# Kernel optimization log

Hardware: AMD Instinct MI355X
Metric: run time of the kernel (lower is better)

The kernel has to match this reference:

```python
import jax, jax.numpy as jnp
import numpy as np

N, C, E, B, NPG, MAX_LEN, H, EF = 16384, 512, 524288, 64, 256, 512, 8, 16
EPS = 1e-5

def layernorm(x, g, b):
    m = jnp.mean(x, axis=-1, keepdims=True)
    v = jnp.mean(jnp.square(x - m), axis=-1, keepdims=True)
    return (x - m) / jnp.sqrt(v + EPS) * g + b

def setup_inputs() -> dict:
    key = jax.random.key(0)
    ks = list(jax.random.split(key, 32))
    x = jax.random.normal(ks[0], (N, C), dtype=jnp.float32)
    edge_attr = jax.random.normal(ks[1], (E, EF), dtype=jnp.float32)
    # edges within each graph of NPG nodes
    src = jax.random.randint(ks[2], (E,), 0, N)
    dst = (src // NPG) * NPG + jax.random.randint(ks[3], (E,), 0, NPG)
    edge_index = jnp.stack([src, dst]).astype(jnp.int64)
    batch = jnp.repeat(jnp.arange(B), NPG).astype(jnp.int64)  # sorted graph ids
    s = 0.03
    p = lambda k, shp: jax.random.normal(k, shp, dtype=jnp.float32) * s
    return dict(
        x=x, edge_attr=edge_attr,
        gcn_w=p(ks[4], (C, C)), gcn_b=jnp.zeros((C,)),
        ep_w=p(ks[5], (EF, C)), ep_b=jnp.zeros((C,)),
        gate_w=p(ks[6], (2 * C, C)), gate_b=jnp.zeros((C,)),
        n1_g=jnp.ones((C,)), n1_b=jnp.zeros((C,)),
        in_w=p(ks[7], (C, 3 * C)), in_b=jnp.zeros((3 * C,)),
        out_w=p(ks[8], (C, C)), out_b=jnp.zeros((C,)),
        tn_g=jnp.ones((C,)), tn_b=jnp.zeros((C,)),
        m_w1=p(ks[9], (C, 2 * C)), m_b1=jnp.zeros((2 * C,)),
        m_w2=p(ks[10], (2 * C, C)), m_b2=jnp.zeros((C,)),
        fn_g=jnp.ones((C,)), fn_b=jnp.zeros((C,)),
        edge_index=edge_index, batch=batch,
    )

def reference(x, edge_attr, gcn_w, gcn_b, ep_w, ep_b, gate_w, gate_b,
              n1_g, n1_b, in_w, in_b, out_w, out_b, tn_g, tn_b,
              m_w1, m_b1, m_w2, m_b2, fn_g, fn_b, edge_index, batch):
    src, dst = edge_index[0], edge_index[1]
    # --- CoGNN: weighted GCN conv (self-loops, sym norm) ---
    ew = jax.lax.stop_gradient(jnp.sqrt(jnp.sum(edge_attr * edge_attr, axis=-1)))
    loop = jnp.arange(N)
    src2 = jnp.concatenate([src, loop]); dst2 = jnp.concatenate([dst, loop])
    ew2 = jnp.concatenate([ew, jnp.ones((N,), ew.dtype)])
    deg = jax.ops.segment_sum(ew2, dst2, num_segments=N)
    dinv = jnp.where(deg > 0, jax.lax.rsqrt(jnp.maximum(deg, 1e-12)), 0.0)
    norm = dinv[src2] * ew2 * dinv[dst2]
    xw = x @ gcn_w
    x_conv = jax.ops.segment_sum(norm[:, None] * xw[src2], dst2, num_segments=N) + gcn_b
    # edge_proj -> scatter_add at source nodes (dropout = identity in eval)
    ef = jax.nn.relu(edge_attr @ ep_w + ep_b)
    ef = jax.ops.segment_sum(ef, src, num_segments=N)
    gate = jax.nn.sigmoid(jnp.concatenate([x_conv, ef], axis=-1) @ gate_w + gate_b)
    x1 = gate * x_conv + (1.0 - gate) * ef
    x1 = jax.nn.relu(layernorm(x1, n1_g, n1_b))
    x = x1 + x  # identity residual (in_channels == hidden_channels)
    # --- to_dense_batch ---
    counts = jax.ops.segment_sum(jnp.ones((N,), jnp.int32), batch, num_segments=B)
    starts = jnp.cumsum(counts) - counts
    pos = jnp.arange(N) - starts[batch]
    xd = jnp.zeros((B, MAX_LEN, C), x.dtype).at[batch, pos].set(x)
    maskd = jnp.zeros((B, MAX_LEN), bool).at[batch, pos].set(True)
    # --- MHA (batch_first, key_padding_mask = ~mask) ---
    Dh = C // H
    qkv = xd @ in_w + in_b
    q, k, v = jnp.split(qkv, 3, axis=-1)
    q = q.reshape(B, MAX_LEN, H, Dh); k = k.reshape(B, MAX_LEN, H, Dh); v = v.reshape(B, MAX_LEN, H, Dh)
    scores = jnp.einsum('blhd,bmhd->bhlm', q, k) / jnp.sqrt(jnp.asarray(Dh, x.dtype))
    scores = jnp.where(maskd[:, None, None, :], scores, -1e9)
    attn = jax.nn.softmax(scores, axis=-1)
    o = jnp.einsum('bhlm,bmhd->blhd', attn, v).reshape(B, MAX_LEN, C)
    o = o @ out_w + out_b
    x_global = o[batch, pos]  # undo dense batching: x_global[mask]
    x = layernorm(x + x_global, tn_g, tn_b)
    # --- MLP ---
    x = x + (jax.nn.silu(x @ m_w1 + m_b1) @ m_w2 + m_b2)
    return layernorm(x, fn_g, fn_b)
```

## Files before the change

kernel.cpp:

```cpp
#include <hip/hip_runtime.h>

#define NN 16384
#define CC 512
#define EE 524288
#define BB 64
#define HH 8
#define EFD 16
#define GEMAXE 10240

typedef __bf16 bf16_t;
typedef __bf16 bf16x4 __attribute__((ext_vector_type(4)));
typedef __bf16 bf16x8 __attribute__((ext_vector_type(8)));
typedef float f32x4v __attribute__((ext_vector_type(4)));

__device__ __forceinline__ float2 ldb2(const bf16_t* p) {
  unsigned w = *(const unsigned*)p;
  return make_float2(__uint_as_float(w << 16), __uint_as_float(w & 0xFFFF0000u));
}

__device__ __forceinline__ int2 xcd_swizzle() {
  int nwg = gridDim.x * gridDim.y;
  int bid = blockIdx.y * gridDim.x + blockIdx.x;
  int wg = (bid & 7) * (nwg >> 3) + (bid >> 3);
  return make_int2(wg % gridDim.x, wg / gridDim.x);
}


__global__ void init_kernel(int* ghist, int* nid_src, bf16_t* eacsr) {
  int i = threadIdx.x;
  if (i < 64) ghist[i] = 0;
  if (i < 32) nid_src[EE + i] = -1;
  ((int*)(eacsr + (size_t)EE * 16))[i] = 0;
}

__global__ __launch_bounds__(256) void edge_pass1(const int* __restrict__ dst,
                                                  int* ghist) {
  __shared__ int h[64];
  int tid = threadIdx.x;
  if (tid < 64) h[tid] = 0;
  __syncthreads();
  int e = blockIdx.x * 256 + tid;
  atomicAdd(&h[dst[e] >> 8], 1);
  __syncthreads();
  if (tid < 64 && h[tid]) atomicAdd(&ghist[tid], h[tid]);
}

__global__ void gexscan_kernel(const int* __restrict__ ghist, int* __restrict__ gstart,
                               int* __restrict__ gcur) {
  if (threadIdx.x == 0) {
    int s = 0;
    for (int g = 0; g < 64; ++g) { gstart[g] = s; gcur[g] = s; s += ghist[g]; }
    gstart[64] = s;
  }
}

__global__ __launch_bounds__(256) void graph_scatter_kernel(
    const int* __restrict__ src, const int* __restrict__ dst,
    const float* __restrict__ ea, int* gcur, int2* __restrict__ grec,
    float* __restrict__ ewg) {
  __shared__ int h[64], base[64], h2[64];
  int tid = threadIdx.x;
  if (tid < 64) { h[tid] = 0; h2[tid] = 0; }
  __syncthreads();
  int e0 = blockIdx.x * 2048;
  int gloc[8];
#pragma unroll
  for (int k = 0; k < 8; ++k) {
    gloc[k] = dst[e0 + k * 256 + tid] >> 8;
    atomicAdd(&h[gloc[k]], 1);
  }
  __syncthreads();
  if (tid < 64) base[tid] = h[tid] ? atomicAdd(&gcur[tid], h[tid]) : 0;
  __syncthreads();
#pragma unroll
  for (int k = 0; k < 8; ++k) {
    int e = e0 + k * 256 + tid;
    int g = gloc[k];
    int p = atomicAdd(&h2[g], 1);
    int pos = base[g] + p;
    int ls = src[e] & 255;
    int ld = dst[e] & 255;
    grec[pos] = make_int2(e | (ls << 19), ld);
    const float4* pa = (const float4*)(ea + (size_t)e * EFD);
    float s = 0.f;
#pragma unroll
    for (int q = 0; q < 4; ++q) {
      float4 v = pa[q];
      s += v.x * v.x + v.y * v.y + v.z * v.z + v.w * v.w;
    }
    ewg[pos] = sqrtf(s);
  }
}

__global__ __launch_bounds__(1024) void graph_sort2_kernel(
    const int2* __restrict__ grec, const float* __restrict__ ewg,
    const int* __restrict__ gstart, int* __restrict__ elist_src,
    int* __restrict__ nid_src, int* __restrict__ start_src,
    float2* __restrict__ dstrec, int* __restrict__ start_dst,
    float* __restrict__ dinv) {
  __shared__ int lbuf[GEMAXE];
  __shared__ unsigned short sl[GEMAXE];
  __shared__ float ewl[GEMAXE];
  __shared__ int h[256], hx[256], h2[256];
  __shared__ float fdinv[256];
  const int g = blockIdx.x & 63;
  const int tid = threadIdx.x;
  const int gs = gstart[g];
  const int cnt = gstart[g + 1] - gs;
  if (tid < 256) { h[tid] = 0; h2[tid] = 0; }
  __syncthreads();
  if (blockIdx.x < 64) {
    for (int i = tid; i < cnt; i += 1024) {
      int2 r = grec[gs + i];
      int ld = r.y;
      sl[i] = (unsigned short)(((r.x >> 19) & 255) | (ld << 8));
      ewl[i] = ewg[gs + i];
      atomicAdd(&h[ld], 1);
    }
    __syncthreads();
    int myc = (tid < 256) ? h[tid] : 0;
    for (int off = 1; off < 256; off <<= 1) {
      int v = (tid < 256 && tid >= off) ? h[tid - off] : 0;
      __syncthreads();
      if (tid < 256) h[tid] += v;
      __syncthreads();
    }
    if (tid < 256) {
      hx[tid] = h[tid] - myc;
      start_dst[g * 256 + tid] = gs + hx[tid];
    }
    if (g == 63 && tid == 0) start_dst[NN] = EE;
    __syncthreads();
    for (int i = tid; i < cnt; i += 1024) {
      int ld = sl[i] >> 8;
      int p = hx[ld] + atomicAdd(&h2[ld], 1);
      lbuf[p] = i;
    }
    __syncthreads();
    if (tid < 256) {
      float dg = 1.0f;
      int s0 = hx[tid], e0 = s0 + myc;
      for (int i = s0; i < e0; ++i) dg += ewl[lbuf[i]];
      float dv = rsqrtf(fmaxf(dg, 1e-12f));
      fdinv[tid] = dv;
      dinv[g * 256 + tid] = dv;
    }
    __syncthreads();
    for (int p = tid; p < cnt; p += 1024) {
      int i = lbuf[p];
      int ls = sl[i] & 255;
      int ld = sl[i] >> 8;
      dstrec[gs + p] =
          make_float2(fdinv[ls] * ewl[i] * fdinv[ld], __int_as_float(ls));
    }
  } else {
    int* wb = (int*)ewl;
    for (int i = tid; i < cnt; i += 1024) {
      int w = grec[gs + i].x;
      wb[i] = w;
      atomicAdd(&h[w >> 19], 1);
    }
    __syncthreads();
    int myc = (tid < 256) ? h[tid] : 0;
    for (int off = 1; off < 256; off <<= 1) {
      int v = (tid < 256 && tid >= off) ? h[tid - off] : 0;
      __syncthreads();
      if (tid < 256) h[tid] += v;
      __syncthreads();
    }
    if (tid < 256) {
      hx[tid] = h[tid] - myc;
      start_src[g * 256 + tid] = gs + hx[tid];
    }
    if (g == 63 && tid == 0) start_src[NN] = EE;
    __syncthreads();
    for (int i = tid; i < cnt; i += 1024) {
      int w = wb[i];
      int ls = w >> 19;
      int p = hx[ls] + atomicAdd(&h2[ls], 1);
      lbuf[p] = w;
    }
    __syncthreads();
    for (int p = tid; p < cnt; p += 1024) {
      int w = lbuf[p];
      elist_src[gs + p] = w & 0x7FFFF;
      nid_src[gs + p] = g * 256 + (w >> 19);
    }
  }
}

__global__ void ea_gather_kernel(const float* __restrict__ ea,
                                 const int* __restrict__ elist,
                                 bf16_t* __restrict__ eacsr) {
  int idx = blockIdx.x * 256 + threadIdx.x;
  if (idx >= EE * 2) return;
  int pos = idx >> 1, half = idx & 1;
  int e = elist[pos];
  const f32x4v* p = (const f32x4v*)(ea + (size_t)e * EFD + half * 8);
  f32x4v u0 = p[0], u1 = p[1];
  bf16x8 f;
#pragma unroll
  for (int r = 0; r < 4; ++r) {
    f[r] = (bf16_t)u0[r];
    f[4 + r] = (bf16_t)u1[r];
  }
  *(bf16x8*)(eacsr + (size_t)pos * 16 + half * 8) = f;
}

__global__ __launch_bounds__(256) void an_build_kernel(
    const float2* __restrict__ dstrec, const int* __restrict__ start_dst,
    const float* __restrict__ dinv, bf16_t* __restrict__ An) {
  __shared__ float AnS[128][256];
  const int g = blockIdx.x >> 1, h = blockIdx.x & 1;
  const int tid = threadIdx.x;
  float4* az = (float4*)&AnS[0][0];
  for (int i = tid; i < 128 * 256 / 4; i += 256)
    az[i] = make_float4(0.f, 0.f, 0.f, 0.f);
  __syncthreads();
  const int nbase = g * 256 + h * 128;
  if (tid < 128) {
    int node = nbase + tid;
    int st = start_dst[node], en = start_dst[node + 1];
    float* row = AnS[tid];
    for (int p = st; p < en; ++p) {
      float2 r = dstrec[p];
      row[__float_as_int(r.y)] += r.x;
    }
    float dv = dinv[node];
    row[h * 128 + tid] += dv * dv;
  }
  __syncthreads();
  bf16_t* out = An + (size_t)nbase * 256;
  const float* s0 = &AnS[0][0];
  for (int i = tid; i < 128 * 256 / 8; i += 256) {
    bf16x8 v;
#pragma unroll
    for (int r = 0; r < 8; ++r) v[r] = (bf16_t)s0[i * 8 + r];
    *(bf16x8*)(out + i * 8) = v;
  }
}


__global__ void cvt_bf16_kernel(const float* __restrict__ in, bf16_t* __restrict__ out,
                                int n4) {
  int i = blockIdx.x * 256 + threadIdx.x;
  if (i >= n4) return;
  float4 v = ((const float4*)in)[i];
  bf16x4 o;
  o[0] = (bf16_t)v.x; o[1] = (bf16_t)v.y; o[2] = (bf16_t)v.z; o[3] = (bf16_t)v.w;
  ((bf16x4*)out)[i] = o;
}

__global__ __launch_bounds__(256) void wt_kernel(const float* __restrict__ W,
                                                 bf16_t* __restrict__ Wt, int K, int N) {
  __shared__ float tile[32][33];
  int bx = blockIdx.x * 32;
  int by = blockIdx.y * 32;
  int tx = threadIdx.x & 31, ty = threadIdx.x >> 5;
#pragma unroll
  for (int i = 0; i < 32; i += 8)
    tile[ty + i][tx] = W[(size_t)(by + ty + i) * N + bx + tx];
  __syncthreads();
#pragma unroll
  for (int i = 0; i < 32; i += 8)
    Wt[(size_t)(bx + ty + i) * K + by + tx] = (bf16_t)tile[tx][ty + i];
}

__global__ __launch_bounds__(512) void ef_mfma_kernel(
    const bf16_t* __restrict__ eacsr, const float* __restrict__ ep_w,
    const float* __restrict__ ep_b, const int* __restrict__ nid,
    const int* __restrict__ start, bf16_t* __restrict__ efb) {
  const int tid = threadIdx.x;
  const int lane = tid & 63;
  const int wv = tid >> 6;
  const int l15 = lane & 15;
  const int g = lane >> 4;
  const int n0 = blockIdx.x * 16;
  const int cbase = wv * 64;

  bf16x8 wfr[4];
#pragma unroll
  for (int t = 0; t < 4; ++t) {
    bf16x8 f = {};
    int c = cbase + t * 16 + l15;
    if (g < 2) {
#pragma unroll
      for (int j = 0; j < 8; ++j) f[j] = (bf16_t)ep_w[(g * 8 + j) * CC + c];
    } else if (g == 2) {
      f[0] = (bf16_t)ep_b[c];
    }
    wfr[t] = f;
  }

  const int st = start[n0];
  const int en = start[n0 + 16];
  const int tgt = n0 + l15;

  f32x4v eacc[4] = {};

  for (int cb = st; cb < en; cb += 32) {
    bf16x8 af[2];
#pragma unroll
    for (int mE = 0; mE < 2; ++mE) {
      bf16x8 f = {};
      if (g < 2) {
        f = *(const bf16x8*)(eacsr + (size_t)(cb + mE * 16 + l15) * 16 + g * 8);
      } else if (g == 2) {
        f[0] = (bf16_t)1.0f;
      }
      af[mE] = f;
    }
    int4 idlo = *(const int4*)(nid + cb + g * 4);
    int4 idhi = *(const int4*)(nid + cb + 16 + g * 4);
    bf16x8 sf;
    sf[0] = (idlo.x == tgt) ? (bf16_t)1.0f : (bf16_t)0.0f;
    sf[1] = (idlo.y == tgt) ? (bf16_t)1.0f : (bf16_t)0.0f;
    sf[2] = (idlo.z == tgt) ? (bf16_t)1.0f : (bf16_t)0.0f;
    sf[3] = (idlo.w == tgt) ? (bf16_t)1.0f : (bf16_t)0.0f;
    sf[4] = (idhi.x == tgt) ? (bf16_t)1.0f : (bf16_t)0.0f;
    sf[5] = (idhi.y == tgt) ? (bf16_t)1.0f : (bf16_t)0.0f;
    sf[6] = (idhi.z == tgt) ? (bf16_t)1.0f : (bf16_t)0.0f;
    sf[7] = (idhi.w == tgt) ? (bf16_t)1.0f : (bf16_t)0.0f;
    __builtin_amdgcn_s_setprio(1);
#pragma unroll
    for (int t = 0; t < 4; ++t) {
      f32x4v s0 = {}, s1 = {};
      s0 = __builtin_amdgcn_mfma_f32_16x16x32_bf16(af[0], wfr[t], s0, 0, 0, 0);
      s1 = __builtin_amdgcn_mfma_f32_16x16x32_bf16(af[1], wfr[t], s1, 0, 0, 0);
      union { bf16x8 v; bf16x4 h[2]; } pf;
#pragma unroll
      for (int r = 0; r < 4; ++r) {
        pf.h[0][r] = (bf16_t)fmaxf(s0[r], 0.f);
        pf.h[1][r] = (bf16_t)fmaxf(s1[r], 0.f);
      }
      eacc[t] = __builtin_amdgcn_mfma_f32_16x16x32_bf16(sf, pf.v, eacc[t], 0, 0, 0);
    }
    __builtin_amdgcn_s_setprio(0);
  }
#pragma unroll
  for (int t = 0; t < 4; ++t) {
    int c = cbase + t * 16 + l15;
#pragma unroll
    for (int r = 0; r < 4; ++r) {
      int node = n0 + g * 4 + r;
      efb[(size_t)node * (2 * CC) + CC + c] = (bf16_t)eacc[t][r];
    }
  }
}

__device__ __forceinline__ void gl_lds16(const bf16_t* g, bf16_t* l) {
  __builtin_amdgcn_global_load_lds(
      (const __attribute__((address_space(1))) void*)g,
      (__attribute__((address_space(3))) void*)l, 16, 0, 0);
}

template <int ACT, int OUT>
__global__ __launch_bounds__(256) void gemm_bf16_kernel(
    const bf16_t* __restrict__ A, const bf16_t* __restrict__ Bt,
    const float* __restrict__ bias, void* __restrict__ Cout, int M, int N, int K) {
  __shared__ __align__(16) bf16_t Al[128 * 64];
  __shared__ __align__(16) bf16_t Bl[128 * 64];
  const int tid = threadIdx.x;
  const int lane = tid & 63;
  const int wave = tid >> 6;
  int2 sw = xcd_swizzle();
  const int row0 = sw.y * 128;
  const int col0 = sw.x * 128;
  const int wm = (wave >> 1) * 64;
  const int wn = (wave & 1) * 64;
  f32x4v acc[4][4] = {};
  const int srow = wave * 8 + (lane >> 3);
  const int sslot = (lane & 7) ^ (lane >> 3);
  const bf16_t* aBase = A + (size_t)(row0 + srow) * K + sslot * 8;
  const bf16_t* bBase = Bt + (size_t)(col0 + srow) * K + sslot * 8;
  const int fr = lane & 15;
  const int g = lane >> 4;
  const int f7 = fr & 7;
  for (int k0 = 0; k0 < K; k0 += 64) {
#pragma unroll
    for (int i = 0; i < 4; ++i)
      gl_lds16(aBase + (size_t)(i * 32) * K + k0, Al + i * 2048 + wave * 512);
#pragma unroll
    for (int i = 0; i < 4; ++i)
      gl_lds16(bBase + (size_t)(i * 32) * K + k0, Bl + i * 2048 + wave * 512);
    __syncthreads();
#pragma unroll
    for (int s = 0; s < 2; ++s) {
      const int sl = ((s * 4 + g) ^ f7) * 8;
      bf16x8 af[4], bfv[4];
#pragma unroll
      for (int m = 0; m < 4; ++m)
        af[m] = *(const bf16x8*)(Al + (wm + m * 16 + fr) * 64 + sl);
#pragma unroll
      for (int n = 0; n < 4; ++n)
        bfv[n] = *(const bf16x8*)(Bl + (wn + n * 16 + fr) * 64 + sl);
#pragma unroll
      for (int m = 0; m < 4; ++m)
#pragma unroll
        for (int n = 0; n < 4; ++n)
          acc[m][n] = __builtin_amdgcn_mfma_f32_16x16x32_bf16(af[m], bfv[n],
                                                              acc[m][n], 0, 0, 0);
    }
    __syncthreads();
  }
  const int fq = (lane >> 4) * 4;
#pragma unroll
  for (int m = 0; m < 4; ++m) {
    int grb = row0 + wm + m * 16 + fq;
#pragma unroll
    for (int n = 0; n < 4; ++n) {
      int gc = col0 + wn + n * 16 + fr;
      float bv = bias ? bias[gc] : 0.f;
#pragma unroll
      for (int r = 0; r < 4; ++r) {
        float v = acc[m][n][r] + bv;
        if (ACT == 1) v = v / (1.f + __expf(-v));
        if (OUT == 0)
          ((float*)Cout)[(size_t)(grb + r) * N + gc] = v;
        else
          ((bf16_t*)Cout)[(size_t)(grb + r) * N + gc] = (bf16_t)v;
      }
    }
  }
}

__global__ __launch_bounds__(256) void an_gemm_kernel(
    const bf16_t* __restrict__ An, const bf16_t* __restrict__ xwT,
    const float* __restrict__ bias, bf16_t* __restrict__ outb) {
  __shared__ __align__(16) bf16_t Al[128 * 64];
  __shared__ __align__(16) bf16_t Bl[128 * 64];
  const int tid = threadIdx.x;
  const int lane = tid & 63;
  const int wave = tid >> 6;
  int2 sw = xcd_swizzle();
  const int row0 = sw.y * 128;
  const int col0 = sw.x * 128;
  const int gr = row0 >> 8;
  f32x4v acc[4][4] = {};
  const int srow = wave * 8 + (lane >> 3);
  const int sslot = (lane & 7) ^ (lane >> 3);
  const bf16_t* aBase = An + (size_t)(row0 + srow) * 256 + sslot * 8;
  const bf16_t* bBase = xwT + (size_t)(col0 + srow) * NN + gr * 256 + sslot * 8;
  const int wm = (wave >> 1) * 64;
  const int wn = (wave & 1) * 64;
  const int fr = lane & 15;
  const int g = lane >> 4;
  const int f7 = fr & 7;
  for (int k0 = 0; k0 < 256; k0 += 64) {
#pragma unroll
    for (int i = 0; i < 4; ++i)
      gl_lds16(aBase + (size_t)(i * 32) * 256 + k0, Al + i * 2048 + wave * 512);
#pragma unroll
    for (int i = 0; i < 4; ++i)
      gl_lds16(bBase + (size_t)(i * 32) * NN + k0, Bl + i * 2048 + wave * 512);
    __syncthreads();
#pragma unroll
    for (int s = 0; s < 2; ++s) {
      const int sl = ((s * 4 + g) ^ f7) * 8;
      bf16x8 af[4], bfv[4];
#pragma unroll
      for (int m = 0; m < 4; ++m)
        af[m] = *(const bf16x8*)(Al + (wm + m * 16 + fr) * 64 + sl);
#pragma unroll
      for (int n = 0; n < 4; ++n)
        bfv[n] = *(const bf16x8*)(Bl + (wn + n * 16 + fr) * 64 + sl);
#pragma unroll
      for (int m = 0; m < 4; ++m)
#pragma unroll
        for (int n = 0; n < 4; ++n)
          acc[m][n] = __builtin_amdgcn_mfma_f32_16x16x32_bf16(af[m], bfv[n],
                                                              acc[m][n], 0, 0, 0);
    }
    __syncthreads();
  }
  const int fq = (lane >> 4) * 4;
#pragma unroll
  for (int m = 0; m < 4; ++m) {
    int grb = row0 + wm + m * 16 + fq;
#pragma unroll
    for (int n = 0; n < 4; ++n) {
      int gc = col0 + wn + n * 16 + fr;
      float bv = bias[gc];
#pragma unroll
      for (int r = 0; r < 4; ++r)
        outb[(size_t)(grb + r) * (2 * CC) + gc] = (bf16_t)(acc[m][n][r] + bv);
    }
  }
}


__device__ inline void block_reduce2(float& s, float& q, float* red) {
#pragma unroll
  for (int off = 32; off >= 1; off >>= 1) {
    s += __shfl_xor(s, off, 64);
    q += __shfl_xor(q, off, 64);
  }
  int wid = threadIdx.x >> 6;
  if ((threadIdx.x & 63) == 0) { red[wid * 2] = s; red[wid * 2 + 1] = q; }
  __syncthreads();
  s = red[0] + red[2] + red[4] + red[6];
  q = red[1] + red[3] + red[5] + red[7];
}

template <int IA, int IB, int WF>
__global__ __launch_bounds__(256) void ln_addT_kernel(
    const void* __restrict__ A, const void* __restrict__ Bv,
    const float* __restrict__ g, const float* __restrict__ be,
    float* __restrict__ outf, bf16_t* __restrict__ outb) {
  int row = blockIdx.x, tid = threadIdx.x, c0 = tid * 2;
  __shared__ float red[8];
  float2 a = IA ? ldb2((const bf16_t*)A + (size_t)row * CC + c0)
                : *(const float2*)((const float*)A + (size_t)row * CC + c0);
  float2 b = IB ? ldb2((const bf16_t*)Bv + (size_t)row * CC + c0)
                : *(const float2*)((const float*)Bv + (size_t)row * CC + c0);
  float x0 = a.x + b.x, x1 = a.y + b.y;
  float s = x0 + x1, q = x0 * x0 + x1 * x1;
  block_reduce2(s, q, red);
  float mean = s * (1.f / CC);
  float var = q * (1.f / CC) - mean * mean;
  float rs = rsqrtf(var + 1e-5f);
  float o0 = (x0 - mean) * rs * g[c0] + be[c0];
  float o1 = (x1 - mean) * rs * g[c0 + 1] + be[c0 + 1];
  if (WF) {
    *(float2*)(outf + (size_t)row * CC + c0) = make_float2(o0, o1);
  } else {
    outb[(size_t)row * CC + c0] = (bf16_t)o0;
    outb[(size_t)row * CC + c0 + 1] = (bf16_t)o1;
  }
}

__global__ __launch_bounds__(256) void ln_gate_kernel(
    const bf16_t* __restrict__ gpreb, const float* __restrict__ gate_b,
    const bf16_t* __restrict__ xcef, const float* __restrict__ n1g,
    const float* __restrict__ n1b, const float* __restrict__ xin,
    bf16_t* __restrict__ x2b) {
  int row = blockIdx.x, tid = threadIdx.x, c0 = tid * 2;
  __shared__ float red[8];
  float2 gp = ldb2(gpreb + (size_t)row * CC + c0);
  float2 xcv = ldb2(xcef + (size_t)row * (2 * CC) + c0);
  float2 efv = ldb2(xcef + (size_t)row * (2 * CC) + CC + c0);
  float g0 = 1.f / (1.f + __expf(-(gp.x + gate_b[c0])));
  float g1 = 1.f / (1.f + __expf(-(gp.y + gate_b[c0 + 1])));
  float x0 = g0 * xcv.x + (1.f - g0) * efv.x;
  float x1 = g1 * xcv.y + (1.f - g1) * efv.y;
  float s = x0 + x1, q = x0 * x0 + x1 * x1;
  block_reduce2(s, q, red);
  float mean = s * (1.f / CC);
  float var = q * (1.f / CC) - mean * mean;
  float rs = rsqrtf(var + 1e-5f);
  float2 xi = *(const float2*)(xin + (size_t)row * CC + c0);
  float o0 = fmaxf((x0 - mean) * rs * n1g[c0] + n1b[c0], 0.f) + xi.x;
  float o1 = fmaxf((x1 - mean) * rs * n1g[c0 + 1] + n1b[c0 + 1], 0.f) + xi.y;
  x2b[(size_t)row * CC + c0] = (bf16_t)o0;
  x2b[(size_t)row * CC + c0 + 1] = (bf16_t)o1;
}

__global__ __launch_bounds__(256) void vt_pack_kernel(const bf16_t* __restrict__ qkvb,
                                                      bf16_t* __restrict__ vt) {
  int b = blockIdx.x >> 3, h = blockIdx.x & 7;
  int nb = b * 256;
  size_t voff = 1024 + (size_t)h * 64;
  char* out = (char*)(vt + (size_t)blockIdx.x * (64 * 256));
  __shared__ bf16_t tile[64][80];
  int tid = threadIdx.x;
  for (int kb = 0; kb < 4; ++kb) {
    __syncthreads();
#pragma unroll
    for (int p = 0; p < 2; ++p) {
      int k = p * 32 + (tid >> 3);
      int d8 = tid & 7;
      bf16x8 v = *(const bf16x8*)(qkvb + (size_t)(nb + kb * 64 + k) * 1536 + voff + d8 * 8);
      *(bf16x8*)(&tile[k][d8 * 8]) = v;
    }
    __syncthreads();
#pragma unroll
    for (int p = 0; p < 2; ++p) {
      int d = p * 32 + (tid >> 3);
      int k8 = tid & 7;
      bf16x8 v;
#pragma unroll
      for (int j = 0; j < 8; ++j) {
        int pos = k8 * 8 + j;
        int sl = pos & 31;
        int srck = (pos & 32) + ((sl >> 3) << 2) + (sl & 3) + (((sl >> 2) & 1) << 4);
        v[j] = tile[srck][d];
      }
      int byteoff = d * 512 + ((kb * 128 + k8 * 16) ^ ((d & 7) << 4));
      *(bf16x8*)(out + byteoff) = v;
    }
  }
}

__global__ __launch_bounds__(256, 2) void attn_mfma_kernel(
    const bf16_t* __restrict__ qkvb, const bf16_t* __restrict__ vt,
    bf16_t* __restrict__ o) {
  const int b = blockIdx.x >> 3;
  const int h = blockIdx.x & 7;
  const int nb = b * 256;
  const int tid = threadIdx.x;
  const int lane = tid & 63;
  const int wv = tid >> 6;
  const int l15 = lane & 15;
  const int g = lane >> 4;
  const int swzk = (l15 & 7) << 4;
  __shared__ __align__(16) bf16_t Klds[256 * 64];
  __shared__ __align__(16) bf16_t Vtlds[64 * 256];
  const size_t qoff = (size_t)h * 64;
  const size_t koff = 512 + (size_t)h * 64;

  {
    const int dcol = 16 * ((tid & 7) ^ ((tid >> 3) & 7));
    const bf16_t* srcb = qkvb + koff + (dcol >> 1);
#pragma unroll
    for (int i = 0; i < 8; ++i) {
      int k = i * 32 + (tid >> 3);
      gl_lds16(srcb + (size_t)(nb + k) * 1536, Klds + ((i * 4096 + wv * 1024) >> 1));
    }
  }
  {
    const bf16_t* vsrc = vt + (size_t)blockIdx.x * (64 * 256);
#pragma unroll
    for (int i = 0; i < 8; ++i) {
      int base = i * 4096 + wv * 1024;
      gl_lds16(vsrc + ((base >> 1) + lane * 8), Vtlds + (base >> 1));
    }
  }

  bf16x8 qf[4][2];
#pragma unroll
  for (int n = 0; n < 4; ++n) {
    const bf16_t* qp = qkvb + (size_t)(nb + wv * 64 + 16 * n + l15) * 1536 + qoff + g * 8;
    qf[n][0] = *(const bf16x8*)(qp);
    qf[n][1] = *(const bf16x8*)(qp + 32);
  }

  __syncthreads();

  f32x4v oacc[4][4] = {};
  float mrun[4] = {-1e30f, -1e30f, -1e30f, -1e30f};
  float lrun[4] = {0.f, 0.f, 0.f, 0.f};

  for (int kc = 0; kc < 4; ++kc) {
    f32x4v sacc[4][4] = {};
    const int kb128 = (kc * 64 + l15) * 128;
    __builtin_amdgcn_s_setprio(1);
#pragma unroll
    for (int m = 0; m < 4; ++m) {
      bf16x8 a0 = *(const bf16x8*)(Klds + ((kb128 + m * 2048 + ((g * 16) ^ swzk)) >> 1));
      bf16x8 a1 =
          *(const bf16x8*)(Klds + ((kb128 + m * 2048 + ((64 + g * 16) ^ swzk)) >> 1));
#pragma unroll
      for (int n = 0; n < 4; ++n) {
        sacc[m][n] = __builtin_amdgcn_mfma_f32_16x16x32_bf16(a0, qf[n][0], sacc[m][n], 0, 0, 0);
        sacc[m][n] = __builtin_amdgcn_mfma_f32_16x16x32_bf16(a1, qf[n][1], sacc[m][n], 0, 0, 0);
      }
    }
    __builtin_amdgcn_s_setprio(0);
    uint2 pb[4][4];
#pragma unroll
    for (int n = 0; n < 4; ++n) {
      float mx = sacc[0][n][0];
#pragma unroll
      for (int m = 0; m < 4; ++m)
#pragma unroll
        for (int r = 0; r < 4; ++r) mx = fmaxf(mx, sacc[m][n][r]);
      mx = fmaxf(mx, __shfl_xor(mx, 16));
      mx = fmaxf(mx, __shfl_xor(mx, 32));
      float mnew = fmaxf(mrun[n], mx);
      float c = __expf((mrun[n] - mnew) * 0.125f);
      mrun[n] = mnew;
      float s = 0.f;
#pragma unroll
      for (int m = 0; m < 4; ++m) {
        float p0 = __expf((sacc[m][n][0] - mnew) * 0.125f);
        float p1 = __expf((sacc[m][n][1] - mnew) * 0.125f);
        float p2 = __expf((sacc[m][n][2] - mnew) * 0.125f);
        float p3 = __expf((sacc[m][n][3] - mnew) * 0.125f);
        s += (p0 + p1) + (p2 + p3);
        union { bf16x4 v; uint2 u; } cv;
        cv.v[0] = (bf16_t)p0; cv.v[1] = (bf16_t)p1;
        cv.v[2] = (bf16_t)p2; cv.v[3] = (bf16_t)p3;
        pb[m][n] = cv.u;
      }
      s += __shfl_xor(s, 16);
      s += __shfl_xor(s, 32);
      lrun[n] = lrun[n] * c + s;
#pragma unroll
      for (int m = 0; m < 4; ++m)
#pragma unroll
        for (int r = 0; r < 4; ++r) oacc[m][n][r] *= c;
    }
    __builtin_amdgcn_s_setprio(1);
#pragma unroll
    for (int h2 = 0; h2 < 2; ++h2) {
      bf16x8 vf[4];
#pragma unroll
      for (int m = 0; m < 4; ++m)
        vf[m] = *(const bf16x8*)(Vtlds + (((16 * m + l15) * 512 +
                                          ((kc * 128 + h2 * 64 + g * 16) ^ swzk)) >> 1));
#pragma unroll
      for (int n = 0; n < 4; ++n) {
        union { uint2 u[2]; bf16x8 v; } pf;
        pf.u[0] = pb[2 * h2][n];
        pf.u[1] = pb[2 * h2 + 1][n];
#pragma unroll
        for (int m = 0; m < 4; ++m)
          oacc[m][n] =
              __builtin_amdgcn_mfma_f32_16x16x32_bf16(vf[m], pf.v, oacc[m][n], 0, 0, 0);
      }
    }
    __builtin_amdgcn_s_setprio(0);
  }
  float inv[4];
#pragma unroll
  for (int n = 0; n < 4; ++n) inv[n] = 1.0f / lrun[n];
#pragma unroll
  for (int m = 0; m < 4; ++m)
#pragma unroll
    for (int n = 0; n < 4; ++n) {
      bf16x4 pk;
#pragma unroll
      for (int r = 0; r < 4; ++r) pk[r] = (bf16_t)(oacc[m][n][r] * inv[n]);
      *(bf16x4*)(o + (size_t)(nb + wv * 64 + 16 * n + l15) * 512 + h * 64 + 16 * m +
                 4 * g) = pk;
    }
}


static inline char* alignp(char* p, size_t a) {
  return (char*)(((uintptr_t)p + a - 1) & ~(uintptr_t)(a - 1));
}

extern "C" void kernel_launch(void* const* d_in, const int* in_sizes, int n_in,
                              void* d_out, int out_size, void* d_ws, size_t ws_size,
                              hipStream_t stream) {
  const float* x = (const float*)d_in[0];
  const float* edge_attr = (const float*)d_in[1];
  const float* gcn_w = (const float*)d_in[2];
  const float* gcn_b = (const float*)d_in[3];
  const float* ep_w = (const float*)d_in[4];
  const float* ep_b = (const float*)d_in[5];
  const float* gate_w = (const float*)d_in[6];
  const float* gate_b = (const float*)d_in[7];
  const float* n1_g = (const float*)d_in[8];
  const float* n1_b = (const float*)d_in[9];
  const float* in_w = (const float*)d_in[10];
  const float* in_b = (const float*)d_in[11];
  const float* out_w = (const float*)d_in[12];
  const float* out_b = (const float*)d_in[13];
  const float* tn_g = (const float*)d_in[14];
  const float* tn_b = (const float*)d_in[15];
  const float* m_w1 = (const float*)d_in[16];
  const float* m_b1 = (const float*)d_in[17];
  const float* m_w2 = (const float*)d_in[18];
  const float* m_b2 = (const float*)d_in[19];
  const float* fn_g = (const float*)d_in[20];
  const float* fn_b = (const float*)d_in[21];
  const int* eidx = (const int*)d_in[22];
  const int* src = eidx;
  const int* dst = eidx + EE;

  float* ws = (float*)d_ws;
  float* R1 = ws;
  float* R2 = R1 + (size_t)NN * 3 * CC;
  float* R3 = R2 + (size_t)NN * CC;
  float* R4 = R3 + (size_t)NN * CC;
  float* dinv = R4 + (size_t)NN * CC;
  int* ip = (int*)(dinv + NN);
  int* ghist = ip;      ip += 64;
  int* gstart = ip;     ip += 65;
  int* gcur = ip;       ip += 64;
  int* elist_src = ip;  ip += EE;
  int* nid_src = ip;    ip += EE + 32;
  int* start_src = ip;  ip += NN + 1;
  int* start_dst = ip;  ip += NN + 1;
  char* bp = alignp((char*)ip, 64);
  int2* grec = (int2*)bp;             bp += (size_t)EE * 8;
  float* ewg = (float*)bp;            bp += (size_t)EE * 4;
  float2* dstrec = (float2*)bp;       bp += (size_t)EE * 8;
  bf16_t* x2b = (bf16_t*)bp;          bp += (size_t)NN * CC * 2;
  bf16_t* gcn_wt = (bf16_t*)bp;       bp += (size_t)CC * CC * 2;
  bf16_t* gate_wt = (bf16_t*)bp;      bp += (size_t)CC * 2 * CC * 2;
  bf16_t* in_wt = (bf16_t*)bp;        bp += (size_t)3 * CC * CC * 2;
  bf16_t* out_wt = (bf16_t*)bp;       bp += (size_t)CC * CC * 2;
  bf16_t* m_w1t = (bf16_t*)bp;        bp += (size_t)2 * CC * CC * 2;
  bf16_t* m_w2t = (bf16_t*)bp;        bp += (size_t)CC * 2 * CC * 2;

  bf16_t* xb = (bf16_t*)R1;
  bf16_t* xcefb = (bf16_t*)R1;
  bf16_t* qkvb = (bf16_t*)R1;
  bf16_t* hb = (bf16_t*)R1;
  bf16_t* eacsr = (bf16_t*)((char*)R1 + (size_t)64 * 1024 * 1024);
  bf16_t* xwT = (bf16_t*)R2;
  bf16_t* gpreb = (bf16_t*)R2;
  bf16_t* ob = (bf16_t*)R2;
  bf16_t* vt = ob + (size_t)NN * CC;
  bf16_t* x3b = (bf16_t*)R2;
  bf16_t* AnFull = (bf16_t*)R3;
  bf16_t* oprjb = (bf16_t*)R4;
  float* yf = R4;

  init_kernel<<<1, 256, 0, stream>>>(ghist, nid_src, eacsr);
  edge_pass1<<<EE / 256, 256, 0, stream>>>(dst, ghist);
  gexscan_kernel<<<1, 64, 0, stream>>>(ghist, gstart, gcur);
  graph_scatter_kernel<<<EE / 2048, 256, 0, stream>>>(src, dst, edge_attr, gcur,
                                                      grec, ewg);
  graph_sort2_kernel<<<128, 1024, 0, stream>>>(grec, ewg, gstart, elist_src, nid_src,
                                               start_src, dstrec, start_dst, dinv);
  ea_gather_kernel<<<(EE * 2 + 255) / 256, 256, 0, stream>>>(edge_attr, elist_src,
                                                             eacsr);
  an_build_kernel<<<128, 256, 0, stream>>>(dstrec, start_dst, dinv, AnFull);

  wt_kernel<<<dim3(CC / 32, CC / 32), 256, 0, stream>>>(gcn_w, gcn_wt, CC, CC);
  wt_kernel<<<dim3(CC / 32, 2 * CC / 32), 256, 0, stream>>>(gate_w, gate_wt, 2 * CC, CC);
  wt_kernel<<<dim3(3 * CC / 32, CC / 32), 256, 0, stream>>>(in_w, in_wt, CC, 3 * CC);
  wt_kernel<<<dim3(CC / 32, CC / 32), 256, 0, stream>>>(out_w, out_wt, CC, CC);
  wt_kernel<<<dim3(2 * CC / 32, CC / 32), 256, 0, stream>>>(m_w1, m_w1t, CC, 2 * CC);
  wt_kernel<<<dim3(CC / 32, 2 * CC / 32), 256, 0, stream>>>(m_w2, m_w2t, 2 * CC, CC);

  cvt_bf16_kernel<<<(NN * CC / 4 + 255) / 256, 256, 0, stream>>>(x, xb, NN * CC / 4);
  gemm_bf16_kernel<0, 1><<<dim3(NN / 128, CC / 128), 256, 0, stream>>>(
      gcn_wt, xb, nullptr, xwT, CC, NN, CC);
  an_gemm_kernel<<<dim3(CC / 128, NN / 128), 256, 0, stream>>>(AnFull, xwT, gcn_b,
                                                               xcefb);
  ef_mfma_kernel<<<NN / 16, 512, 0, stream>>>(eacsr, ep_w, ep_b, nid_src, start_src,
                                              xcefb);
  dim3 gA(CC / 128, NN / 128);
  gemm_bf16_kernel<0, 1><<<gA, 256, 0, stream>>>(xcefb, gate_wt, nullptr, gpreb, NN,
                                                 CC, 2 * CC);
  ln_gate_kernel<<<NN, 256, 0, stream>>>(gpreb, gate_b, xcefb, n1_g, n1_b, x, x2b);

  dim3 gQ(3 * CC / 128, NN / 128);
  gemm_bf16_kernel<0, 1><<<gQ, 256, 0, stream>>>(x2b, in_wt, in_b, qkvb, NN, 3 * CC, CC);
  vt_pack_kernel<<<BB * HH, 256, 0, stream>>>(qkvb, vt);
  attn_mfma_kernel<<<BB * HH, 256, 0, stream>>>(qkvb, vt, ob);
  gemm_bf16_kernel<0, 1><<<gA, 256, 0, stream>>>(ob, out_wt, out_b, oprjb, NN, CC, CC);
  ln_addT_kernel<1, 1, 0><<<NN, 256, 0, stream>>>(x2b, oprjb, tn_g, tn_b, nullptr, x3b);

  dim3 gH(2 * CC / 128, NN / 128);
  gemm_bf16_kernel<1, 1><<<gH, 256, 0, stream>>>(x3b, m_w1t, m_b1, hb, NN, 2 * CC, CC);
  gemm_bf16_kernel<0, 0><<<gA, 256, 0, stream>>>(hb, m_w2t, m_b2, yf, NN, CC, 2 * CC);
  ln_addT_kernel<1, 0, 1><<<NN, 256, 0, stream>>>(x3b, yf, fn_g, fn_b, (float*)d_out,
                                                  nullptr);
}
```

Measured before the change: 443.4 us.

## Use 8-wave GEMM blocks and 128-thread vectorized layernorm kernels

All bf16 GEMM kernels, including the normalized-adjacency GEMM, now launch 512 threads (8 waves) per 128x128 tile. Each wave computes a 32x64 sub-tile with half the accumulators, and the LDS fill is spread across all threads. The aim is more latency hiding per tile and fewer registers per wave, at the cost of more LDS fragment reads per MFMA. The layernorm and gate kernels move to 128 threads with 4-wide vectorized loads and stores to cut reduction and launch overhead per row.

Measured after the change: 416.7 us. -6.0%, faster.

```diff
diff --git a/kernel.cpp b/kernel.cpp
--- a/kernel.cpp
+++ b/kernel.cpp
@@ -16,6 +16,12 @@
 __device__ __forceinline__ float2 ldb2(const bf16_t* p) {
   unsigned w = *(const unsigned*)p;
   return make_float2(__uint_as_float(w << 16), __uint_as_float(w & 0xFFFF0000u));
+}
+
+__device__ __forceinline__ float4 ldb4(const bf16_t* p) {
+  uint2 w = *(const uint2*)p;
+  return make_float4(__uint_as_float(w.x << 16), __uint_as_float(w.x & 0xFFFF0000u),
+                     __uint_as_float(w.y << 16), __uint_as_float(w.y & 0xFFFF0000u));
 }
 
 __device__ __forceinline__ int2 xcd_swizzle() {
@@ -355,7 +361,7 @@
 }
 
 template <int ACT, int OUT>
-__global__ __launch_bounds__(256) void gemm_bf16_kernel(
+__global__ __launch_bounds__(512) void gemm_bf16_kernel(
     const bf16_t* __restrict__ A, const bf16_t* __restrict__ Bt,
     const float* __restrict__ bias, void* __restrict__ Cout, int M, int N, int K) {
   __shared__ __align__(16) bf16_t Al[128 * 64];
@@ -366,36 +372,34 @@
   int2 sw = xcd_swizzle();
   const int row0 = sw.y * 128;
   const int col0 = sw.x * 128;
-  const int wm = (wave >> 1) * 64;
-  const int wn = (wave & 1) * 64;
-  f32x4v acc[4][4] = {};
-  const int srow = wave * 8 + (lane >> 3);
-  const int sslot = (lane & 7) ^ (lane >> 3);
+  const int wm = wave >> 1;
+  const int wn = wave & 1;
+  f32x4v acc[2][4] = {};
+  const int srow = tid >> 3;
+  const int sslot = (tid & 7) ^ (srow & 7);
   const bf16_t* aBase = A + (size_t)(row0 + srow) * K + sslot * 8;
   const bf16_t* bBase = Bt + (size_t)(col0 + srow) * K + sslot * 8;
   const int fr = lane & 15;
   const int g = lane >> 4;
   const int f7 = fr & 7;
   for (int k0 = 0; k0 < K; k0 += 64) {
-#pragma unroll
-    for (int i = 0; i < 4; ++i)
-      gl_lds16(aBase + (size_t)(i * 32) * K + k0, Al + i * 2048 + wave * 512);
-#pragma unroll
-    for (int i = 0; i < 4; ++i)
-      gl_lds16(bBase + (size_t)(i * 32) * K + k0, Bl + i * 2048 + wave * 512);
+    gl_lds16(aBase + k0, Al + tid * 8);
+    gl_lds16(aBase + (size_t)64 * K + k0, Al + 4096 + tid * 8);
+    gl_lds16(bBase + k0, Bl + tid * 8);
+    gl_lds16(bBase + (size_t)64 * K + k0, Bl + 4096 + tid * 8);
     __syncthreads();
 #pragma unroll
     for (int s = 0; s < 2; ++s) {
       const int sl = ((s * 4 + g) ^ f7) * 8;
-      bf16x8 af[4], bfv[4];
-#pragma unroll
-      for (int m = 0; m < 4; ++m)
-        af[m] = *(const bf16x8*)(Al + (wm + m * 16 + fr) * 64 + sl);
+      bf16x8 af[2], bfv[4];
+#pragma unroll
+      for (int m = 0; m < 2; ++m)
+        af[m] = *(const bf16x8*)(Al + (wm * 32 + m * 16 + fr) * 64 + sl);
 #pragma unroll
       for (int n = 0; n < 4; ++n)
-        bfv[n] = *(const bf16x8*)(Bl + (wn + n * 16 + fr) * 64 + sl);
-#pragma unroll
-      for (int m = 0; m < 4; ++m)
+        bfv[n] = *(const bf16x8*)(Bl + (wn * 64 + n * 16 + fr) * 64 + sl);
+#pragma unroll
+      for (int m = 0; m < 2; ++m)
 #pragma unroll
         for (int n = 0; n < 4; ++n)
           acc[m][n] = __builtin_amdgcn_mfma_f32_16x16x32_bf16(af[m], bfv[n],
@@ -405,11 +409,11 @@
   }
   const int fq = (lane >> 4) * 4;
 #pragma unroll
-  for (int m = 0; m < 4; ++m) {
-    int grb = row0 + wm + m * 16 + fq;
+  for (int m = 0; m < 2; ++m) {
+    int grb = row0 + wm * 32 + m * 16 + fq;
 #pragma unroll
     for (int n = 0; n < 4; ++n) {
-      int gc = col0 + wn + n * 16 + fr;
+      int gc = col0 + wn * 64 + n * 16 + fr;
       float bv = bias ? bias[gc] : 0.f;
 #pragma unroll
       for (int r = 0; r < 4; ++r) {
@@ -424,7 +428,7 @@
   }
 }
 
-__global__ __launch_bounds__(256) void an_gemm_kernel(
+__global__ __launch_bounds__(512) void an_gemm_kernel(
     const bf16_t* __restrict__ An, const bf16_t* __restrict__ xwT,
     const float* __restrict__ bias, bf16_t* __restrict__ outb) {
   __shared__ __align__(16) bf16_t Al[128 * 64];
@@ -436,36 +440,34 @@
   const int row0 = sw.y * 128;
   const int col0 = sw.x * 128;
   const int gr = row0 >> 8;
-  f32x4v acc[4][4] = {};
-  const int srow = wave * 8 + (lane >> 3);
-  const int sslot = (lane & 7) ^ (lane >> 3);
+  const int wm = wave >> 1;
+  const int wn = wave & 1;
+  f32x4v acc[2][4] = {};
+  const int srow = tid >> 3;
+  const int sslot = (tid & 7) ^ (srow & 7);
   const bf16_t* aBase = An + (size_t)(row0 + srow) * 256 + sslot * 8;
   const bf16_t* bBase = xwT + (size_t)(col0 + srow) * NN + gr * 256 + sslot * 8;
-  const int wm = (wave >> 1) * 64;
-  const int wn = (wave & 1) * 64;
   const int fr = lane & 15;
   const int g = lane >> 4;
   const int f7 = fr & 7;
   for (int k0 = 0; k0 < 256; k0 += 64) {
-#pragma unroll
-    for (int i = 0; i < 4; ++i)
-      gl_lds16(aBase + (size_t)(i * 32) * 256 + k0, Al + i * 2048 + wave * 512);
-#pragma unroll
-    for (int i = 0; i < 4; ++i)
-      gl_lds16(bBase + (size_t)(i * 32) * NN + k0, Bl + i * 2048 + wave * 512);
+    gl_lds16(aBase + k0, Al + tid * 8);
+    gl_lds16(aBase + (size_t)64 * 256 + k0, Al + 4096 + tid * 8);
+    gl_lds16(bBase + k0, Bl + tid * 8);
+    gl_lds16(bBase + (size_t)64 * NN + k0, Bl + 4096 + tid * 8);
     __syncthreads();
 #pragma unroll
     for (int s = 0; s < 2; ++s) {
       const int sl = ((s * 4 + g) ^ f7) * 8;
-      bf16x8 af[4], bfv[4];
-#pragma unroll
-      for (int m = 0; m < 4; ++m)
-        af[m] = *(const bf16x8*)(Al + (wm + m * 16 + fr) * 64 + sl);
+      bf16x8 af[2], bfv[4];
+#pragma unroll
+      for (int m = 0; m < 2; ++m)
+        af[m] = *(const bf16x8*)(Al + (wm * 32 + m * 16 + fr) * 64 + sl);
 #pragma unroll
       for (int n = 0; n < 4; ++n)
-        bfv[n] = *(const bf16x8*)(Bl + (wn + n * 16 + fr) * 64 + sl);
-#pragma unroll
-      for (int m = 0; m < 4; ++m)
+        bfv[n] = *(const bf16x8*)(Bl + (wn * 64 + n * 16 + fr) * 64 + sl);
+#pragma unroll
+      for (int m = 0; m < 2; ++m)
 #pragma unroll
         for (int n = 0; n < 4; ++n)
           acc[m][n] = __builtin_amdgcn_mfma_f32_16x16x32_bf16(af[m], bfv[n],
@@ -475,11 +477,11 @@
   }
   const int fq = (lane >> 4) * 4;
 #pragma unroll
-  for (int m = 0; m < 4; ++m) {
-    int grb = row0 + wm + m * 16 + fq;
+  for (int m = 0; m < 2; ++m) {
+    int grb = row0 + wm * 32 + m * 16 + fq;
 #pragma unroll
     for (int n = 0; n < 4; ++n) {
-      int gc = col0 + wn + n * 16 + fr;
+      int gc = col0 + wn * 64 + n * 16 + fr;
       float bv = bias[gc];
 #pragma unroll
       for (int r = 0; r < 4; ++r)
@@ -489,7 +491,7 @@
 }
 
 
-__device__ inline void block_reduce2(float& s, float& q, float* red) {
+__device__ inline void block_reduce2_2w(float& s, float& q, float* red) {
 #pragma unroll
   for (int off = 32; off >= 1; off >>= 1) {
     s += __shfl_xor(s, off, 64);
@@ -498,61 +500,78 @@
   int wid = threadIdx.x >> 6;
   if ((threadIdx.x & 63) == 0) { red[wid * 2] = s; red[wid * 2 + 1] = q; }
   __syncthreads();
-  s = red[0] + red[2] + red[4] + red[6];
-  q = red[1] + red[3] + red[5] + red[7];
+  s = red[0] + red[2];
+  q = red[1] + red[3];
 }
 
 template <int IA, int IB, int WF>
-__global__ __launch_bounds__(256) void ln_addT_kernel(
+__global__ __launch_bounds__(128) void ln_addT_kernel(
     const void* __restrict__ A, const void* __restrict__ Bv,
     const float* __restrict__ g, const float* __restrict__ be,
     float* __restrict__ outf, bf16_t* __restrict__ outb) {
-  int row = blockIdx.x, tid = threadIdx.x, c0 = tid * 2;
-  __shared__ float red[8];
-  float2 a = IA ? ldb2((const bf16_t*)A + (size_t)row * CC + c0)
-                : *(const float2*)((const float*)A + (size_t)row * CC + c0);
-  float2 b = IB ? ldb2((const bf16_t*)Bv + (size_t)row * CC + c0)
-                : *(const float2*)((const float*)Bv + (size_t)row * CC + c0);
-  float x0 = a.x + b.x, x1 = a.y + b.y;
-  float s = x0 + x1, q = x0 * x0 + x1 * x1;
-  block_reduce2(s, q, red);
+  int row = blockIdx.x, tid = threadIdx.x, c0 = tid * 4;
+  __shared__ float red[4];
+  float4 a = IA ? ldb4((const bf16_t*)A + (size_t)row * CC + c0)
+                : *(const float4*)((const float*)A + (size_t)row * CC + c0);
+  float4 b = IB ? ldb4((const bf16_t*)Bv + (size_t)row * CC + c0)
+                : *(const float4*)((const float*)Bv + (size_t)row * CC + c0);
+  float x0 = a.x + b.x, x1 = a.y + b.y, x2 = a.z + b.z, x3 = a.w + b.w;
+  float s = (x0 + x1) + (x2 + x3);
+  float q = (x0 * x0 + x1 * x1) + (x2 * x2 + x3 * x3);
+  block_reduce2_2w(s, q, red);
   float mean = s * (1.f / CC);
   float var = q * (1.f / CC) - mean * mean;
   float rs = rsqrtf(var + 1e-5f);
-  float o0 = (x0 - mean) * rs * g[c0] + be[c0];
-  float o1 = (x1 - mean) * rs * g[c0 + 1] + be[c0 + 1];
+  float4 gg = *(const float4*)(g + c0);
+  float4 bb = *(const float4*)(be + c0);
+  float o0 = (x0 - mean) * rs * gg.x + bb.x;
+  float o1 = (x1 - mean) * rs * gg.y + bb.y;
+  float o2 = (x2 - mean) * rs * gg.z + bb.z;
+  float o3 = (x3 - mean) * rs * gg.w + bb.w;
   if (WF) {
-    *(float2*)(outf + (size_t)row * CC + c0) = make_float2(o0, o1);
+    *(float4*)(outf + (size_t)row * CC + c0) = make_float4(o0, o1, o2, o3);
   } else {
-    outb[(size_t)row * CC + c0] = (bf16_t)o0;
-    outb[(size_t)row * CC + c0 + 1] = (bf16_t)o1;
-  }
-}
-
-__global__ __launch_bounds__(256) void ln_gate_kernel(
+    bf16x4 pk;
+    pk[0] = (bf16_t)o0; pk[1] = (bf16_t)o1; pk[2] = (bf16_t)o2; pk[3] = (bf16_t)o3;
+    *(bf16x4*)(outb + (size_t)row * CC + c0) = pk;
+  }
+}
+
+__global__ __launch_bounds__(128) void ln_gate_kernel(
     const bf16_t* __restrict__ gpreb, const float* __restrict__ gate_b,
     const bf16_t* __restrict__ xcef, const float* __restrict__ n1g,
     const float* __restrict__ n1b, const float* __restrict__ xin,
     bf16_t* __restrict__ x2b) {
-  int row = blockIdx.x, tid = threadIdx.x, c0 = tid * 2;
-  __shared__ float red[8];
-  float2 gp = ldb2(gpreb + (size_t)row * CC + c0);
-  float2 xcv = ldb2(xcef + (size_t)row * (2 * CC) + c0);
-  float2 efv = ldb2(xcef + (size_t)row * (2 * CC) + CC + c0);
-  float g0 = 1.f / (1.f + __expf(-(gp.x + gate_b[c0])));
-  float g1 = 1.f / (1.f + __expf(-(gp.y + gate_b[c0 + 1])));
+  int row = blockIdx.x, tid = threadIdx.x, c0 = tid * 4;
+  __shared__ float red[4];
+  float4 gp = ldb4(gpreb + (size_t)row * CC + c0);
+  float4 xcv = ldb4(xcef + (size_t)row * (2 * CC) + c0);
+  float4 efv = ldb4(xcef + (size_t)row * (2 * CC) + CC + c0);
+  float4 gb = *(const float4*)(gate_b + c0);
+  float g0 = 1.f / (1.f + __expf(-(gp.x + gb.x)));
+  float g1 = 1.f / (1.f + __expf(-(gp.y + gb.y)));
+  float g2 = 1.f / (1.f + __expf(-(gp.z + gb.z)));
+  float g3 = 1.f / (1.f + __expf(-(gp.w + gb.w)));
   float x0 = g0 * xcv.x + (1.f - g0) * efv.x;
   float x1 = g1 * xcv.y + (1.f - g1) * efv.y;
-  float s = x0 + x1, q = x0 * x0 + x1 * x1;
-  block_reduce2(s, q, red);
+  float x2 = g2 * xcv.z + (1.f - g2) * efv.z;
+  float x3 = g3 * xcv.w + (1.f - g3) * efv.w;
+  float s = (x0 + x1) + (x2 + x3);
+  float q = (x0 * x0 + x1 * x1) + (x2 * x2 + x3 * x3);
+  block_reduce2_2w(s, q, red);
   float mean = s * (1.f / CC);
   float var = q * (1.f / CC) - mean * mean;
   float rs = rsqrtf(var + 1e-5f);
-  float2 xi = *(const float2*)(xin + (size_t)row * CC + c0);
-  float o0 = fmaxf((x0 - mean) * rs * n1g[c0] + n1b[c0], 0.f) + xi.x;
-  float o1 = fmaxf((x1 - mean) * rs * n1g[c0 + 1] + n1b[c0 + 1], 0.f) + xi.y;
-  x2b[(size_t)row * CC + c0] = (bf16_t)o0;
-  x2b[(size_t)row * CC + c0 + 1] = (bf16_t)o1;
+  float4 ng = *(const float4*)(n1g + c0);
+  float4 nb = *(const float4*)(n1b + c0);
+  float4 xi = *(const float4*)(xin + (size_t)row * CC + c0);
+  float o0 = fmaxf((x0 - mean) * rs * ng.x + nb.x, 0.f) + xi.x;
+  float o1 = fmaxf((x1 - mean) * rs * ng.y + nb.y, 0.f) + xi.y;
+  float o2 = fmaxf((x2 - mean) * rs * ng.z + nb.z, 0.f) + xi.z;
+  float o3 = fmaxf((x3 - mean) * rs * ng.w + nb.w, 0.f) + xi.w;
+  bf16x4 pk;
+  pk[0] = (bf16_t)o0; pk[1] = (bf16_t)o1; pk[2] = (bf16_t)o2; pk[3] = (bf16_t)o3;
+  *(bf16x4*)(x2b + (size_t)row * CC + c0) = pk;
 }
 
 __global__ __launch_bounds__(256) void vt_pack_kernel(const bf16_t* __restrict__ qkvb,
@@ -819,27 +838,27 @@
   wt_kernel<<<dim3(CC / 32, 2 * CC / 32), 256, 0, stream>>>(m_w2, m_w2t, 2 * CC, CC);
 
   cvt_bf16_kernel<<<(NN * CC / 4 + 255) / 256, 256, 0, stream>>>(x, xb, NN * CC / 4);
-  gemm_bf16_kernel<0, 1><<<dim3(NN / 128, CC / 128), 256, 0, stream>>>(
+  gemm_bf16_kernel<0, 1><<<dim3(NN / 128, CC / 128), 512, 0, stream>>>(
       gcn_wt, xb, nullptr, xwT, CC, NN, CC);
-  an_gemm_kernel<<<dim3(CC / 128, NN / 128), 256, 0, stream>>>(AnFull, xwT, gcn_b,
+  an_gemm_kernel<<<dim3(CC / 128, NN / 128), 512, 0, stream>>>(AnFull, xwT, gcn_b,
                                                                xcefb);
   ef_mfma_kernel<<<NN / 16, 512, 0, stream>>>(eacsr, ep_w, ep_b, nid_src, start_src,
                                               xcefb);
   dim3 gA(CC / 128, NN / 128);
-  gemm_bf16_kernel<0, 1><<<gA, 256, 0, stream>>>(xcefb, gate_wt, nullptr, gpreb, NN,
+  gemm_bf16_kernel<0, 1><<<gA, 512, 0, stream>>>(xcefb, gate_wt, nullptr, gpreb, NN,
                                                  CC, 2 * CC);
-  ln_gate_kernel<<<NN, 256, 0, stream>>>(gpreb, gate_b, xcefb, n1_g, n1_b, x, x2b);
+  ln_gate_kernel<<<NN, 128, 0, stream>>>(gpreb, gate_b, xcefb, n1_g, n1_b, x, x2b);
 
   dim3 gQ(3 * CC / 128, NN / 128);
-  gemm_bf16_kernel<0, 1><<<gQ, 256, 0, stream>>>(x2b, in_wt, in_b, qkvb, NN, 3 * CC, CC);
+  gemm_bf16_kernel<0, 1><<<gQ, 512, 0, stream>>>(x2b, in_wt, in_b, qkvb, NN, 3 * CC, CC);
   vt_pack_kernel<<<BB * HH, 256, 0, stream>>>(qkvb, vt);
   attn_mfma_kernel<<<BB * HH, 256, 0, stream>>>(qkvb, vt, ob);
-  gemm_bf16_kernel<0, 1><<<gA, 256, 0, stream>>>(ob, out_wt, out_b, oprjb, NN, CC, CC);
-  ln_addT_kernel<1, 1, 0><<<NN, 256, 0, stream>>>(x2b, oprjb, tn_g, tn_b, nullptr, x3b);
+  gemm_bf16_kernel<0, 1><<<gA, 512, 0, stream>>>(ob, out_wt, out_b, oprjb, NN, CC, CC);
+  ln_addT_kernel<1, 1, 0><<<NN, 128, 0, stream>>>(x2b, oprjb, tn_g, tn_b, nullptr, x3b);
 
   dim3 gH(2 * CC / 128, NN / 128);
-  gemm_bf16_kernel<1, 1><<<gH, 256, 0, stream>>>(x3b, m_w1t, m_b1, hb, NN, 2 * CC, CC);
-  gemm_bf16_kernel<0, 0><<<gA, 256, 0, stream>>>(hb, m_w2t, m_b2, yf, NN, CC, 2 * CC);
-  ln_addT_kernel<1, 0, 1><<<NN, 256, 0, stream>>>(x3b, yf, fn_g, fn_b, (float*)d_out,
+  gemm_bf16_kernel<1, 1><<<gH, 512, 0, stream>>>(x3b, m_w1t, m_b1, hb, NN, 2 * CC, CC);
+  gemm_bf16_kernel<0, 0><<<gA, 512, 0, stream>>>(hb, m_w2t, m_b2, yf, NN, CC, 2 * CC);
+  ln_addT_kernel<1, 0, 1><<<NN, 128, 0, stream>>>(x3b, yf, fn_g, fn_b, (float*)d_out,
                                                   nullptr);
 }
```
